# Optimization experiments

Hardware: AMD Instinct MI355X
Metric: run time of the kernel (lower is better)

The kernel has to match this reference:

```python
import jax, jax.numpy as jnp
import numpy as np

B, S, D, H = 4, 2048, 512, 8
HD = D // H


def setup_inputs() -> dict:
    key = jax.random.key(0)
    ks = jax.random.split(key, 12)
    x = jax.random.normal(ks[0], (B, S, D), dtype=jnp.float32)
    docking_scores = jax.random.uniform(ks[1], (B, S), dtype=jnp.float32)
    mask = jax.random.randint(ks[2], (B, S), 0, 2).astype(jnp.bool_)
    s = 0.02
    Wq = jax.random.normal(ks[3], (D, D), dtype=jnp.float32) * s
    bq = jnp.zeros((D,), dtype=jnp.float32)
    Wk = jax.random.normal(ks[4], (D, D), dtype=jnp.float32) * s
    bk = jnp.zeros((D,), dtype=jnp.float32)
    Wv = jax.random.normal(ks[5], (D, D), dtype=jnp.float32) * s
    bv = jnp.zeros((D,), dtype=jnp.float32)
    Wo = jax.random.normal(ks[6], (D, D), dtype=jnp.float32) * s
    bo = jnp.zeros((D,), dtype=jnp.float32)
    alpha = jnp.float32(0.5)
    beta = jnp.float32(0.5)
    return {"x": x, "docking_scores": docking_scores, "mask": mask,
            "Wq": Wq, "bq": bq, "Wk": Wk, "bk": bk, "Wv": Wv, "bv": bv,
            "Wo": Wo, "bo": bo, "alpha": alpha, "beta": beta}


def reference(x, docking_scores, mask, Wq, bq, Wk, bk, Wv, bv, Wo, bo, alpha, beta):
    # daa_type == ATTENTION: attention + docking-score blend (alpha unused here).
    b, s, d = x.shape
    # zero docking scores at padded positions; shape (B, S, 1)
    ds = jnp.where(mask[..., None], docking_scores[..., None], 0.0)
    def proj(W, bias):
        return (jnp.einsum('bsd,ed->bse', x, W) + bias).reshape(b, s, H, HD).transpose(0, 2, 1, 3)
    Q = proj(Wq, bq)  # (B, H, S, HD)
    K = proj(Wk, bk)
    V = proj(Wv, bv)
    scores = jnp.einsum('bhqd,bhkd->bhqk', Q, K) / jnp.sqrt(jnp.float32(HD))
    scores = jnp.where(mask[:, None, None, :], scores, -jnp.inf)  # key-padding mask
    attn = jax.nn.softmax(scores, axis=-1)  # (B, H, S, S)
    # docking blend: (B,1,S,1) broadcasts over heads and key dim (faithful to torch expand)
    attn = (1.0 - beta) * attn + beta * ds[:, None, :, :]
    ctx = jnp.einsum('bhqk,bhkd->bhqd', attn, V)
    ctx = ctx.transpose(0, 2, 1, 3).reshape(b, s, d)
    return jnp.einsum('bsd,od->bso', ctx, Wo) + bo
```

## Files before the change

kernel.cpp:

```cpp
#include <hip/hip_runtime.h>
#include <hip/hip_bf16.h>

#define B_ 4
#define S_ 2048
#define D_ 512
#define H_ 8
#define HD_ 64

typedef unsigned int uint;
typedef unsigned short ushort_t;
typedef __attribute__((ext_vector_type(4))) float f32x4;
typedef __attribute__((ext_vector_type(8))) short bf16x8;

#if __has_builtin(__builtin_amdgcn_exp2f)
#define EXP2F __builtin_amdgcn_exp2f
#else
#define EXP2F exp2f
#endif

__device__ __forceinline__ float bf2f(unsigned short u){ union{uint i;float f;}c; c.i = (uint)u<<16; return c.f; }
__device__ __forceinline__ unsigned short f2bf(float f){
    __hip_bfloat16 h = __float2bfloat16(f);
    return *reinterpret_cast<unsigned short*>(&h);
}

__device__ __forceinline__ void gload16(const unsigned short* g, const ushort_t* l){
    __builtin_amdgcn_global_load_lds(
        (const __attribute__((address_space(1))) unsigned int*)g,
        (__attribute__((address_space(3))) unsigned int*)l, 16, 0, 0);
}

__global__ __launch_bounds__(256) void convert_all(
    const float* __restrict__ x,
    const float* __restrict__ Wq, const float* __restrict__ Wk,
    const float* __restrict__ Wv, const float* __restrict__ Wo,
    ushort_t* __restrict__ xb, ushort_t* __restrict__ Wqkvb, ushort_t* __restrict__ Wob)
{
    const int NX = 1048576;
    const int NW = 65536;
    const int total = NX + 4 * NW;
    for (int i = blockIdx.x * 256 + threadIdx.x; i < total; i += gridDim.x * 256) {
        const float* src; ushort_t* dst; int so, dofs;
        if (i < NX) { src = x; so = i; dst = xb; dofs = i; }
        else if (i < NX + 3 * NW) {
            int j = i - NX;
            if (j < NW)          { src = Wq; so = j; }
            else if (j < 2 * NW) { src = Wk; so = j - NW; }
            else                 { src = Wv; so = j - 2 * NW; }
            dst = Wqkvb; dofs = j;
        } else { int k = i - NX - 3 * NW; src = Wo; so = k; dst = Wob; dofs = k; }
        float4 v = ((const float4*)src)[so];
        ushort4 u;
        u.x = f2bf(v.x); u.y = f2bf(v.y); u.z = f2bf(v.z); u.w = f2bf(v.w);
        ((ushort4*)dst)[dofs] = u;
    }
}

template<int MODE>
__global__ __launch_bounds__(256) void gemm_mfma(
    const ushort_t* __restrict__ A, const ushort_t* __restrict__ Bw,
    const float* __restrict__ b0, const float* __restrict__ b1, const float* __restrict__ b2,
    ushort_t* __restrict__ O0, ushort_t* __restrict__ O1, ushort_t* __restrict__ O2,
    float* __restrict__ Of)
{
    __shared__ __align__(16) unsigned char smem[34816];
    ushort_t* sA = (ushort_t*)smem;
    ushort_t* sB = sA + 8192;

    const int t = threadIdx.x, w = t >> 6, l = t & 63, g = l >> 4, c = l & 15;
    const int wm = w >> 1, wn = w & 1;
    const int row0 = blockIdx.y * 128, col0 = blockIdx.x * 128;

    const ushort_t* aSrc[4]; const ushort_t* bSrc[4];
    ushort_t* aDst[4]; ushort_t* bDst[4];
    #pragma unroll
    for (int i = 0; i < 4; ++i) {
        int cc = i * 256 + t;
        int row = cc >> 3, slot = (cc & 7) ^ (row & 7);
        aSrc[i] = A  + (size_t)(row0 + row) * 512 + slot * 8;
        bSrc[i] = Bw + (size_t)(col0 + row) * 512 + slot * 8;
        aDst[i] = sA + (i * 256 + w * 64) * 8;
        bDst[i] = sB + (i * 256 + w * 64) * 8;
    }

    f32x4 acc[4][4];
    #pragma unroll
    for (int mi = 0; mi < 4; ++mi)
        #pragma unroll
        for (int ni = 0; ni < 4; ++ni) acc[mi][ni] = (f32x4)0.f;

    for (int ks = 0; ks < 8; ++ks) {
        #pragma unroll
        for (int i = 0; i < 4; ++i) {
            gload16(aSrc[i], aDst[i]);
            gload16(bSrc[i], bDst[i]);
        }
        __syncthreads();
        #pragma unroll
        for (int kh = 0; kh < 2; ++kh) {
            bf16x8 af[4], bfv[4];
            const int sw = (((kh << 2) | g) ^ (c & 7)) << 3;
            #pragma unroll
            for (int mi = 0; mi < 4; ++mi)
                af[mi] = *(const bf16x8*)&sA[(wm * 64 + mi * 16 + c) * 64 + sw];
            #pragma unroll
            for (int ni = 0; ni < 4; ++ni)
                bfv[ni] = *(const bf16x8*)&sB[(wn * 64 + ni * 16 + c) * 64 + sw];
            #pragma unroll
            for (int mi = 0; mi < 4; ++mi)
                #pragma unroll
                for (int ni = 0; ni < 4; ++ni)
                    acc[mi][ni] = __builtin_amdgcn_mfma_f32_16x16x32_bf16(af[mi], bfv[ni], acc[mi][ni], 0, 0, 0);
        }
        #pragma unroll
        for (int i = 0; i < 4; ++i) { aSrc[i] += 64; bSrc[i] += 64; }
        __syncthreads();
    }

    if (MODE == 1) {
        #pragma unroll
        for (int mi = 0; mi < 4; ++mi)
            #pragma unroll
            for (int ni = 0; ni < 4; ++ni) {
                int n = col0 + wn * 64 + ni * 16 + c;
                float bias = b0[n];
                #pragma unroll
                for (int r = 0; r < 4; ++r)
                    Of[(size_t)(row0 + wm * 64 + mi * 16 + 4 * g + r) * 512 + n] =
                        acc[mi][ni][r] + bias;
            }
    } else {
        const int which = col0 >> 9;
        const float* bias = which == 0 ? b0 : (which == 1 ? b1 : b2);
        ushort_t (*Cl)[136] = (ushort_t(*)[136])smem;
        if (which < 2) {
            #pragma unroll
            for (int mi = 0; mi < 4; ++mi)
                #pragma unroll
                for (int ni = 0; ni < 4; ++ni) {
                    int n = wn * 64 + ni * 16 + c;
                    float bb = bias[(col0 & 511) + n];
                    #pragma unroll
                    for (int r = 0; r < 4; ++r)
                        Cl[wm * 64 + mi * 16 + 4 * g + r][n] = f2bf(acc[mi][ni][r] + bb);
                }
        } else {
            #pragma unroll
            for (int mi = 0; mi < 4; ++mi)
                #pragma unroll
                for (int ni = 0; ni < 4; ++ni) {
                    int n = wn * 64 + ni * 16 + c;
                    float bb = bias[(col0 & 511) + n];
                    #pragma unroll
                    for (int r = 0; r < 4; ++r)
                        Cl[n][wm * 64 + mi * 16 + 4 * g + r] = f2bf(acc[mi][ni][r] + bb);
                }
        }
        __syncthreads();
        const int r = t >> 1, half = t & 1;
        const int b = row0 >> 11;
        if (which < 2) {
            ushort_t* Out = which == 0 ? O0 : O1;
            int s = (row0 & 2047) + r;
            int e = (col0 & 511) + half * 64;
            int h = e >> 6;
            ushort_t* dst = Out + (((size_t)(b * 8 + h) * 2048 + s) << 6);
            #pragma unroll
            for (int j = 0; j < 8; ++j)
                *(bf16x8*)(dst + j * 8) = *(const bf16x8*)&Cl[r][half * 64 + j * 8];
        } else {
            int e = (col0 & 511) + r;
            int h = e >> 6, d = e & 63;
            int s0 = (row0 & 2047) + half * 64;
            ushort_t* dst = O2 + ((size_t)(b * 8 + h) * 64 + d) * 2048 + s0;
            #pragma unroll
            for (int j = 0; j < 8; ++j)
                *(bf16x8*)(dst + j * 8) = *(const bf16x8*)&Cl[r][half * 64 + j * 8];
        }
    }
}

__global__ __launch_bounds__(256) void vsum2(
    const __hip_bfloat16* __restrict__ Vt, float* __restrict__ Vsum)
{
    const int row = blockIdx.x * 4 + (threadIdx.x >> 6);
    const int l = threadIdx.x & 63;
    const unsigned short* p = (const unsigned short*)Vt + (size_t)row * S_;
    float s = 0.f;
    #pragma unroll
    for (int i = 0; i < 4; ++i) {
        uint4 u = *(const uint4*)(p + i * 512 + l * 8);
        s += bf2f((unsigned short)(u.x & 0xffff)) + bf2f((unsigned short)(u.x >> 16));
        s += bf2f((unsigned short)(u.y & 0xffff)) + bf2f((unsigned short)(u.y >> 16));
        s += bf2f((unsigned short)(u.z & 0xffff)) + bf2f((unsigned short)(u.z >> 16));
        s += bf2f((unsigned short)(u.w & 0xffff)) + bf2f((unsigned short)(u.w >> 16));
    }
    #pragma unroll
    for (int m = 1; m < 64; m <<= 1) s += __shfl_xor(s, m);
    if (l == 0) Vsum[row] = s;
}

__global__ __launch_bounds__(256, 2) void attn_mfma(
    const __hip_bfloat16* __restrict__ Qb, const __hip_bfloat16* __restrict__ Kb,
    const __hip_bfloat16* __restrict__ Vt, const float* __restrict__ Vsum,
    const float* __restrict__ dock, const int* __restrict__ mask,
    const float* __restrict__ beta_p, ushort_t* __restrict__ ctxb)
{
    __shared__ __align__(16) unsigned char smem[59392];
    ushort_t* Kbuf = (ushort_t*)smem;
    ushort_t* Vbuf = (ushort_t*)(smem + 16384);
    ushort_t (*Plds)[32][72] = (ushort_t(*)[32][72])(smem + 32768);
    float* mbias = (float*)(smem + 51200);
    float (*ctxl)[32][68] = (float(*)[32][68])smem;

    const int flat = blockIdx.x;
    const int xcd = flat & 7, idx = flat >> 3;
    const int bh = ((idx >> 4) << 3) + xcd;
    const int qtile = idx & 15;
    const int b = bh >> 3, h = bh & 7;
    const int t = threadIdx.x, w = t >> 6, l = t & 63;
    const int g = l >> 4, c = l & 15;
    const int q0 = qtile * 128 + w * 32;
    const float beta = beta_p[0];
    const ushort_t* Kp = (const ushort_t*)Kb + (size_t)bh * S_ * HD_;
    const ushort_t* Vp = (const ushort_t*)Vt + (size_t)bh * HD_ * S_;

    int koff[2], voff[2];
    const ushort_t* kdst[2]; const ushort_t* vdst[2];
    {
        const int srow = t >> 3, sslot = t & 7;
        #pragma unroll
        for (int ch = 0; ch < 2; ++ch) {
            int row = ch * 32 + srow;
            int sl = ((sslot ^ (row & 7))) * 8;
            koff[ch] = row * 64 + sl;
            voff[ch] = row * 2048 + sl;
            kdst[ch] = Kbuf + (ch * 256 + w * 64) * 8;
            vdst[ch] = Vbuf + (ch * 256 + w * 64) * 8;
        }
    }
#define STAGE(PAR, K0N) do {                                                    \
    _Pragma("unroll")                                                           \
    for (int ch = 0; ch < 2; ++ch) {                                            \
        gload16(Kp + (size_t)(K0N) * 64 + koff[ch], kdst[ch] + (PAR) * 4096);   \
        gload16(Vp + (K0N) + voff[ch],              vdst[ch] + (PAR) * 4096);   \
    }                                                                           \
} while (0)

    for (int i = t; i < 2048; i += 256)
        mbias[i] = mask[b * S_ + i] ? 0.f : -1e30f;
    STAGE(0, 0);

    bf16x8 qf[2][2];
    #pragma unroll
    for (int qt = 0; qt < 2; ++qt)
        #pragma unroll
        for (int ks = 0; ks < 2; ++ks) {
            const unsigned short* qp = (const unsigned short*)Qb +
                ((size_t)bh * S_ + q0 + qt * 16 + c) * HD_ + ks * 32 + g * 8;
            bf16x8 raw = *(const bf16x8*)qp;
            bf16x8 sc8;
            #pragma unroll
            for (int j = 0; j < 8; ++j) {
                float f = bf2f((unsigned short)raw[j]) * 0.125f;
                sc8[j] = (short)f2bf(f);
            }
            qf[qt][ks] = sc8;
        }

    f32x4 cacc[2][4];
    #pragma unroll
    for (int qt = 0; qt < 2; ++qt)
        #pragma unroll
        for (int dt = 0; dt < 4; ++dt) cacc[qt][dt] = (f32x4)0.f;
    float l_[2] = {0.f, 0.f};

    const int fsw0 = (g ^ (c & 7)) * 8;
    const int fsw1 = ((4 | g) ^ (c & 7)) * 8;

    __syncthreads();

    for (int k0 = 0, par = 0; k0 < S_; k0 += 64, par ^= 1) {
        if (k0 + 64 < S_) STAGE(par ^ 1, k0 + 64);
        const ushort_t* KB = Kbuf + par * 4096;
        const ushort_t* VB = Vbuf + par * 4096;

        bf16x8 kf[8];
        #pragma unroll
        for (int kt = 0; kt < 4; ++kt) {
            const ushort_t* kr = KB + (kt * 16 + c) * 64;
            kf[kt * 2]     = *(const bf16x8*)(kr + fsw0);
            kf[kt * 2 + 1] = *(const bf16x8*)(kr + fsw1);
        }
        bf16x8 vf[8];
        #pragma unroll
        for (int dt = 0; dt < 4; ++dt) {
            const ushort_t* vr = VB + (dt * 16 + c) * 64;
            vf[dt * 2]     = *(const bf16x8*)(vr + fsw0);
            vf[dt * 2 + 1] = *(const bf16x8*)(vr + fsw1);
        }

        f32x4 sacc[2][4];
        #pragma unroll
        for (int qt = 0; qt < 2; ++qt)
            #pragma unroll
            for (int kt = 0; kt < 4; ++kt) sacc[qt][kt] = (f32x4)0.f;
        __builtin_amdgcn_s_setprio(1);
        #pragma unroll
        for (int kt = 0; kt < 4; ++kt)
            #pragma unroll
            for (int qt = 0; qt < 2; ++qt) {
                sacc[qt][kt] = __builtin_amdgcn_mfma_f32_16x16x32_bf16(kf[kt * 2],     qf[qt][0], sacc[qt][kt], 0, 0, 0);
                sacc[qt][kt] = __builtin_amdgcn_mfma_f32_16x16x32_bf16(kf[kt * 2 + 1], qf[qt][1], sacc[qt][kt], 0, 0, 0);
            }
        __builtin_amdgcn_s_setprio(0);

        float mb_[4][4];
        #pragma unroll
        for (int kt = 0; kt < 4; ++kt)
            #pragma unroll
            for (int r = 0; r < 4; ++r)
                mb_[kt][r] = mbias[k0 + kt * 16 + g * 4 + r];

        #pragma unroll
        for (int qt = 0; qt < 2; ++qt) {
            float p_[16];
            float ps = 0.f;
            #pragma unroll
            for (int kt = 0; kt < 4; ++kt)
                #pragma unroll
                for (int r = 0; r < 4; ++r) {
                    float v = fmaf(sacc[qt][kt][r], 1.4426950408889634f, mb_[kt][r]);
                    float p = EXP2F(v);
                    p_[kt * 4 + r] = p;
                    ps += p;
                }
            l_[qt] += ps;
            #pragma unroll
            for (int kt = 0; kt < 4; ++kt) {
                uint lo = (uint)f2bf(p_[kt * 4 + 0]) | ((uint)f2bf(p_[kt * 4 + 1]) << 16);
                uint hi = (uint)f2bf(p_[kt * 4 + 2]) | ((uint)f2bf(p_[kt * 4 + 3]) << 16);
                *(uint2*)&Plds[w][16 * qt + c][kt * 16 + g * 4] = make_uint2(lo, hi);
            }
        }
        asm volatile("s_waitcnt lgkmcnt(0)" ::: "memory");
        __builtin_amdgcn_sched_barrier(0);

        bf16x8 pf[2][2];
        #pragma unroll
        for (int qt = 0; qt < 2; ++qt)
            #pragma unroll
            for (int ks = 0; ks < 2; ++ks)
                pf[qt][ks] = *(const bf16x8*)&Plds[w][16 * qt + c][ks * 32 + g * 8];
        __builtin_amdgcn_s_setprio(1);
        #pragma unroll
        for (int dt = 0; dt < 4; ++dt)
            #pragma unroll
            for (int qt = 0; qt < 2; ++qt) {
                cacc[qt][dt] = __builtin_amdgcn_mfma_f32_16x16x32_bf16(vf[dt * 2],     pf[qt][0], cacc[qt][dt], 0, 0, 0);
                cacc[qt][dt] = __builtin_amdgcn_mfma_f32_16x16x32_bf16(vf[dt * 2 + 1], pf[qt][1], cacc[qt][dt], 0, 0, 0);
            }
        __builtin_amdgcn_s_setprio(0);
        __syncthreads();
    }
#undef STAGE

    #pragma unroll
    for (int qt = 0; qt < 2; ++qt) {
        l_[qt] += __shfl_xor(l_[qt], 16);
        l_[qt] += __shfl_xor(l_[qt], 32);
    }

    __syncthreads();

    #pragma unroll
    for (int qt = 0; qt < 2; ++qt) {
        int qg = q0 + 16 * qt + c;
        float w1 = (1.f - beta) / l_[qt];
        float dq = (mask[b * S_ + qg] ? dock[b * S_ + qg] : 0.f) * beta;
        #pragma unroll
        for (int dt = 0; dt < 4; ++dt)
            #pragma unroll
            for (int r = 0; r < 4; ++r) {
                int d = dt * 16 + g * 4 + r;
                ctxl[w][16 * qt + c][d] = cacc[qt][dt][r] * w1 + dq * Vsum[bh * 64 + d];
            }
    }
    asm volatile("s_waitcnt lgkmcnt(0)" ::: "memory");
    __builtin_amdgcn_sched_barrier(0);
    {
        const int qloc = l >> 1, half = l & 1;
        const int qg = q0 + qloc;
        ushort_t* cp = ctxb + ((size_t)(b * 2048 + qg)) * 512 + h * 64 + half * 32;
        #pragma unroll
        for (int j = 0; j < 4; ++j) {
            float4 v0 = *(const float4*)&ctxl[w][qloc][half * 32 + j * 8];
            float4 v1 = *(const float4*)&ctxl[w][qloc][half * 32 + j * 8 + 4];
            bf16x8 u;
            u[0] = (short)f2bf(v0.x); u[1] = (short)f2bf(v0.y);
            u[2] = (short)f2bf(v0.z); u[3] = (short)f2bf(v0.w);
            u[4] = (short)f2bf(v1.x); u[5] = (short)f2bf(v1.y);
            u[6] = (short)f2bf(v1.z); u[7] = (short)f2bf(v1.w);
            *(bf16x8*)(cp + j * 8) = u;
        }
    }
}

extern "C" void kernel_launch(void* const* d_in, const int* in_sizes, int n_in,
                              void* d_out, int out_size, void* d_ws, size_t ws_size,
                              hipStream_t stream)
{
    const float* x    = (const float*)d_in[0];
    const float* dock = (const float*)d_in[1];
    const int*   mask = (const int*)d_in[2];
    const float* Wq   = (const float*)d_in[3];
    const float* bq   = (const float*)d_in[4];
    const float* Wk   = (const float*)d_in[5];
    const float* bk   = (const float*)d_in[6];
    const float* Wv   = (const float*)d_in[7];
    const float* bv   = (const float*)d_in[8];
    const float* Wo   = (const float*)d_in[9];
    const float* bo   = (const float*)d_in[10];
    const float* beta = (const float*)d_in[12];
    float* out = (float*)d_out;

    const size_t nqkv = (size_t)B_ * H_ * S_ * HD_;
    ushort_t* xb    = (ushort_t*)d_ws;
    ushort_t* Qb    = xb + nqkv;
    ushort_t* Kb    = Qb + nqkv;
    ushort_t* Vt    = Kb + nqkv;
    ushort_t* Wqkvb = Vt + nqkv;
    ushort_t* Wob   = Wqkvb + 1536 * 512;
    float*    Vsum  = (float*)(Wob + 512 * 512);
    ushort_t* ctxb  = xb;

    convert_all<<<1280, 256, 0, stream>>>(x, Wq, Wk, Wv, Wo, xb, Wqkvb, Wob);
    gemm_mfma<0><<<dim3(12, 64), 256, 0, stream>>>(xb, Wqkvb, bq, bk, bv, Qb, Kb, Vt, nullptr);
    vsum2<<<512, 256, 0, stream>>>((const __hip_bfloat16*)Vt, Vsum);
    attn_mfma<<<512, 256, 0, stream>>>(
        (const __hip_bfloat16*)Qb, (const __hip_bfloat16*)Kb, (const __hip_bfloat16*)Vt,
        Vsum, dock, mask, beta, ctxb);
    gemm_mfma<1><<<dim3(4, 64), 256, 0, stream>>>(ctxb, Wob, bo, nullptr, nullptr,
                                                  nullptr, nullptr, nullptr, out);
}
```

Measured before the change: 108.8 us.

## Switch attention to 32x32x16 MFMA with register-resident P and global mask bias

Rewrites the attention inner loop to use 32x32x16 bf16 MFMAs. The S accumulator layout now matches the B-operand layout of the PV MFMA, so P stays in registers and no longer round-trips through LDS. The 1/sqrt(d) scale is folded into the exp2 constant instead of pre-scaling Q, and the mask bias is precomputed once in the convert kernel and read from global memory, which shrinks LDS use. The risks are higher register pressure from the 16-wide accumulators, and V fragments now need split 8-byte LDS reads with possible bank conflicts.

```diff
diff --git a/kernel.cpp b/kernel.cpp
--- a/kernel.cpp
+++ b/kernel.cpp
@@ -10,6 +10,7 @@
 typedef unsigned int uint;
 typedef unsigned short ushort_t;
 typedef __attribute__((ext_vector_type(4))) float f32x4;
+typedef __attribute__((ext_vector_type(16))) float f32x16;
 typedef __attribute__((ext_vector_type(8))) short bf16x8;
 
 #if __has_builtin(__builtin_amdgcn_exp2f)
@@ -34,7 +35,9 @@
     const float* __restrict__ x,
     const float* __restrict__ Wq, const float* __restrict__ Wk,
     const float* __restrict__ Wv, const float* __restrict__ Wo,
-    ushort_t* __restrict__ xb, ushort_t* __restrict__ Wqkvb, ushort_t* __restrict__ Wob)
+    const int* __restrict__ mask,
+    ushort_t* __restrict__ xb, ushort_t* __restrict__ Wqkvb, ushort_t* __restrict__ Wob,
+    float* __restrict__ mbg)
 {
     const int NX = 1048576;
     const int NW = 65536;
@@ -54,6 +57,15 @@
         u.x = f2bf(v.x); u.y = f2bf(v.y); u.z = f2bf(v.z); u.w = f2bf(v.w);
         ((ushort4*)dst)[dofs] = u;
     }
+    for (int i = blockIdx.x * 256 + threadIdx.x; i < 2048; i += gridDim.x * 256) {
+        int4 mv = ((const int4*)mask)[i];
+        float4 o;
+        o.x = mv.x ? 0.f : -1e30f;
+        o.y = mv.y ? 0.f : -1e30f;
+        o.z = mv.z ? 0.f : -1e30f;
+        o.w = mv.w ? 0.f : -1e30f;
+        ((float4*)mbg)[i] = o;
+    }
 }
 
 template<int MODE>
@@ -204,26 +216,26 @@
     const __hip_bfloat16* __restrict__ Qb, const __hip_bfloat16* __restrict__ Kb,
     const __hip_bfloat16* __restrict__ Vt, const float* __restrict__ Vsum,
     const float* __restrict__ dock, const int* __restrict__ mask,
-    const float* __restrict__ beta_p, ushort_t* __restrict__ ctxb)
+    const float* __restrict__ mbg, const float* __restrict__ beta_p,
+    ushort_t* __restrict__ ctxb)
 {
-    __shared__ __align__(16) unsigned char smem[59392];
+    __shared__ __align__(16) unsigned char smem[35328];
     ushort_t* Kbuf = (ushort_t*)smem;
     ushort_t* Vbuf = (ushort_t*)(smem + 16384);
-    ushort_t (*Plds)[32][72] = (ushort_t(*)[32][72])(smem + 32768);
-    float* mbias = (float*)(smem + 51200);
-    float (*ctxl)[32][68] = (float(*)[32][68])smem;
 
     const int flat = blockIdx.x;
     const int xcd = flat & 7, idx = flat >> 3;
     const int bh = ((idx >> 4) << 3) + xcd;
     const int qtile = idx & 15;
-    const int b = bh >> 3, h = bh & 7;
-    const int t = threadIdx.x, w = t >> 6, l = t & 63;
-    const int g = l >> 4, c = l & 15;
+    const int b = bh >> 3, h8 = bh & 7;
+    const int t = threadIdx.x, w = t >> 6, lam = t & 63;
+    const int lq = lam & 31, hf = lam >> 5;
     const int q0 = qtile * 128 + w * 32;
+    const int qg = q0 + lq;
     const float beta = beta_p[0];
     const ushort_t* Kp = (const ushort_t*)Kb + (size_t)bh * S_ * HD_;
     const ushort_t* Vp = (const ushort_t*)Vt + (size_t)bh * HD_ * S_;
+    const float* mbp = mbg + b * S_;
 
     int koff[2], voff[2];
     const ushort_t* kdst[2]; const ushort_t* vdst[2];
@@ -232,7 +244,7 @@
         #pragma unroll
         for (int ch = 0; ch < 2; ++ch) {
             int row = ch * 32 + srow;
-            int sl = ((sslot ^ (row & 7))) * 8;
+            int sl = (sslot ^ (row & 7)) * 8;
             koff[ch] = row * 64 + sl;
             voff[ch] = row * 2048 + sl;
             kdst[ch] = Kbuf + (ch * 256 + w * 64) * 8;
@@ -247,36 +259,19 @@
     }                                                                           \
 } while (0)
 
-    for (int i = t; i < 2048; i += 256)
-        mbias[i] = mask[b * S_ + i] ? 0.f : -1e30f;
     STAGE(0, 0);
 
-    bf16x8 qf[2][2];
+    bf16x8 qf[4];
     #pragma unroll
-    for (int qt = 0; qt < 2; ++qt)
-        #pragma unroll
-        for (int ks = 0; ks < 2; ++ks) {
-            const unsigned short* qp = (const unsigned short*)Qb +
-                ((size_t)bh * S_ + q0 + qt * 16 + c) * HD_ + ks * 32 + g * 8;
-            bf16x8 raw = *(const bf16x8*)qp;
-            bf16x8 sc8;
-            #pragma unroll
-            for (int j = 0; j < 8; ++j) {
-                float f = bf2f((unsigned short)raw[j]) * 0.125f;
-                sc8[j] = (short)f2bf(f);
-            }
-            qf[qt][ks] = sc8;
-        }
-
-    f32x4 cacc[2][4];
-    #pragma unroll
-    for (int qt = 0; qt < 2; ++qt)
-        #pragma unroll
-        for (int dt = 0; dt < 4; ++dt) cacc[qt][dt] = (f32x4)0.f;
-    float l_[2] = {0.f, 0.f};
-
-    const int fsw0 = (g ^ (c & 7)) * 8;
-    const int fsw1 = ((4 | g) ^ (c & 7)) * 8;
+    for (int hd = 0; hd < 4; ++hd)
+        qf[hd] = *(const bf16x8*)((const ushort_t*)Qb +
+                 ((size_t)bh * S_ + qg) * HD_ + hd * 16 + hf * 8);
+
+    f32x16 cacc[2];
+    cacc[0] = (f32x16)0.f;
+    cacc[1] = (f32x16)0.f;
+    float l_ = 0.f;
+    const float CSC = 0.18033688011112042f;
 
     __syncthreads();
 
@@ -285,113 +280,95 @@
         const ushort_t* KB = Kbuf + par * 4096;
         const ushort_t* VB = Vbuf + par * 4096;
 
-        bf16x8 kf[8];
-        #pragma unroll
-        for (int kt = 0; kt < 4; ++kt) {
-            const ushort_t* kr = KB + (kt * 16 + c) * 64;
-            kf[kt * 2]     = *(const bf16x8*)(kr + fsw0);
-            kf[kt * 2 + 1] = *(const bf16x8*)(kr + fsw1);
-        }
-        bf16x8 vf[8];
-        #pragma unroll
-        for (int dt = 0; dt < 4; ++dt) {
-            const ushort_t* vr = VB + (dt * 16 + c) * 64;
-            vf[dt * 2]     = *(const bf16x8*)(vr + fsw0);
-            vf[dt * 2 + 1] = *(const bf16x8*)(vr + fsw1);
-        }
-
-        f32x4 sacc[2][4];
-        #pragma unroll
-        for (int qt = 0; qt < 2; ++qt)
-            #pragma unroll
-            for (int kt = 0; kt < 4; ++kt) sacc[qt][kt] = (f32x4)0.f;
+        f32x16 sacc[2];
+        sacc[0] = (f32x16)0.f;
+        sacc[1] = (f32x16)0.f;
         __builtin_amdgcn_s_setprio(1);
         #pragma unroll
-        for (int kt = 0; kt < 4; ++kt)
-            #pragma unroll
-            for (int qt = 0; qt < 2; ++qt) {
-                sacc[qt][kt] = __builtin_amdgcn_mfma_f32_16x16x32_bf16(kf[kt * 2],     qf[qt][0], sacc[qt][kt], 0, 0, 0);
-                sacc[qt][kt] = __builtin_amdgcn_mfma_f32_16x16x32_bf16(kf[kt * 2 + 1], qf[qt][1], sacc[qt][kt], 0, 0, 0);
+        for (int kt2 = 0; kt2 < 2; ++kt2) {
+            const int krow = kt2 * 32 + lq;
+            const ushort_t* kr = KB + krow * 64;
+            const int krs = krow & 7;
+            #pragma unroll
+            for (int hd = 0; hd < 4; ++hd) {
+                bf16x8 kf = *(const bf16x8*)(kr + ((((hd << 1) | hf) ^ krs) << 3));
+                sacc[kt2] = __builtin_amdgcn_mfma_f32_32x32x16_bf16(kf, qf[hd], sacc[kt2], 0, 0, 0);
             }
+        }
         __builtin_amdgcn_s_setprio(0);
 
-        float mb_[4][4];
-        #pragma unroll
-        for (int kt = 0; kt < 4; ++kt)
-            #pragma unroll
-            for (int r = 0; r < 4; ++r)
-                mb_[kt][r] = mbias[k0 + kt * 16 + g * 4 + r];
-
-        #pragma unroll
-        for (int qt = 0; qt < 2; ++qt) {
-            float p_[16];
-            float ps = 0.f;
-            #pragma unroll
-            for (int kt = 0; kt < 4; ++kt)
-                #pragma unroll
-                for (int r = 0; r < 4; ++r) {
-                    float v = fmaf(sacc[qt][kt][r], 1.4426950408889634f, mb_[kt][r]);
-                    float p = EXP2F(v);
-                    p_[kt * 4 + r] = p;
-                    ps += p;
+        float p[2][16];
+        #pragma unroll
+        for (int kt2 = 0; kt2 < 2; ++kt2) {
+            #pragma unroll
+            for (int qd = 0; qd < 4; ++qd) {
+                float4 mb = *(const float4*)(mbp + k0 + kt2 * 32 + qd * 8 + hf * 4);
+                float pv0 = EXP2F(fmaf(sacc[kt2][qd * 4 + 0], CSC, mb.x));
+                float pv1 = EXP2F(fmaf(sacc[kt2][qd * 4 + 1], CSC, mb.y));
+                float pv2 = EXP2F(fmaf(sacc[kt2][qd * 4 + 2], CSC, mb.z));
+                float pv3 = EXP2F(fmaf(sacc[kt2][qd * 4 + 3], CSC, mb.w));
+                p[kt2][qd * 4 + 0] = pv0; p[kt2][qd * 4 + 1] = pv1;
+                p[kt2][qd * 4 + 2] = pv2; p[kt2][qd * 4 + 3] = pv3;
+                l_ += pv0 + pv1 + pv2 + pv3;
+            }
+        }
+
+        __builtin_amdgcn_s_setprio(1);
+        #pragma unroll
+        for (int kt2 = 0; kt2 < 2; ++kt2) {
+            #pragma unroll
+            for (int ks = 0; ks < 2; ++ks) {
+                bf16x8 pf;
+                #pragma unroll
+                for (int m = 0; m < 8; ++m)
+                    pf[m] = (short)f2bf(p[kt2][ks * 8 + m]);
+                const int gB = (kt2 << 2) + (ks << 1);
+                #pragma unroll
+                for (int dt = 0; dt < 2; ++dt) {
+                    const int vrow = dt * 32 + lq;
+                    const int vrs = vrow & 7;
+                    const ushort_t* vr = VB + vrow * 64;
+                    uint2 lo = *(const uint2*)(vr + (((gB    ) ^ vrs) << 3) + (hf << 2));
+                    uint2 hi = *(const uint2*)(vr + (((gB + 1) ^ vrs) << 3) + (hf << 2));
+                    union { bf16x8 v; uint4 u; } cv;
+                    cv.u = make_uint4(lo.x, lo.y, hi.x, hi.y);
+                    cacc[dt] = __builtin_amdgcn_mfma_f32_32x32x16_bf16(cv.v, pf, cacc[dt], 0, 0, 0);
                 }
-            l_[qt] += ps;
-            #pragma unroll
-            for (int kt = 0; kt < 4; ++kt) {
-                uint lo = (uint)f2bf(p_[kt * 4 + 0]) | ((uint)f2bf(p_[kt * 4 + 1]) << 16);
-                uint hi = (uint)f2bf(p_[kt * 4 + 2]) | ((uint)f2bf(p_[kt * 4 + 3]) << 16);
-                *(uint2*)&Plds[w][16 * qt + c][kt * 16 + g * 4] = make_uint2(lo, hi);
             }
         }
-        asm volatile("s_waitcnt lgkmcnt(0)" ::: "memory");
-        __builtin_amdgcn_sched_barrier(0);
-
-        bf16x8 pf[2][2];
-        #pragma unroll
-        for (int qt = 0; qt < 2; ++qt)
-            #pragma unroll
-            for (int ks = 0; ks < 2; ++ks)
-                pf[qt][ks] = *(const bf16x8*)&Plds[w][16 * qt + c][ks * 32 + g * 8];
-        __builtin_amdgcn_s_setprio(1);
-        #pragma unroll
-        for (int dt = 0; dt < 4; ++dt)
-            #pragma unroll
-            for (int qt = 0; qt < 2; ++qt) {
-                cacc[qt][dt] = __builtin_amdgcn_mfma_f32_16x16x32_bf16(vf[dt * 2],     pf[qt][0], cacc[qt][dt], 0, 0, 0);
-                cacc[qt][dt] = __builtin_amdgcn_mfma_f32_16x16x32_bf16(vf[dt * 2 + 1], pf[qt][1], cacc[qt][dt], 0, 0, 0);
-            }
         __builtin_amdgcn_s_setprio(0);
         __syncthreads();
     }
 #undef STAGE
 
-    #pragma unroll
-    for (int qt = 0; qt < 2; ++qt) {
-        l_[qt] += __shfl_xor(l_[qt], 16);
-        l_[qt] += __shfl_xor(l_[qt], 32);
-    }
+    l_ += __shfl_xor(l_, 32);
 
     __syncthreads();
 
-    #pragma unroll
-    for (int qt = 0; qt < 2; ++qt) {
-        int qg = q0 + 16 * qt + c;
-        float w1 = (1.f - beta) / l_[qt];
+    float (*ctxl)[32][68] = (float(*)[32][68])smem;
+    {
+        float w1 = (1.f - beta) / l_;
         float dq = (mask[b * S_ + qg] ? dock[b * S_ + qg] : 0.f) * beta;
         #pragma unroll
-        for (int dt = 0; dt < 4; ++dt)
-            #pragma unroll
-            for (int r = 0; r < 4; ++r) {
-                int d = dt * 16 + g * 4 + r;
-                ctxl[w][16 * qt + c][d] = cacc[qt][dt][r] * w1 + dq * Vsum[bh * 64 + d];
+        for (int dt = 0; dt < 2; ++dt)
+            #pragma unroll
+            for (int qd = 0; qd < 4; ++qd) {
+                int d0 = dt * 32 + qd * 8 + hf * 4;
+                float4 vs = *(const float4*)(Vsum + bh * 64 + d0);
+                float4 o;
+                o.x = cacc[dt][qd * 4 + 0] * w1 + dq * vs.x;
+                o.y = cacc[dt][qd * 4 + 1] * w1 + dq * vs.y;
+                o.z = cacc[dt][qd * 4 + 2] * w1 + dq * vs.z;
+                o.w = cacc[dt][qd * 4 + 3] * w1 + dq * vs.w;
+                *(float4*)&ctxl[w][lq][d0] = o;
             }
     }
     asm volatile("s_waitcnt lgkmcnt(0)" ::: "memory");
     __builtin_amdgcn_sched_barrier(0);
     {
-        const int qloc = l >> 1, half = l & 1;
-        const int qg = q0 + qloc;
-        ushort_t* cp = ctxb + ((size_t)(b * 2048 + qg)) * 512 + h * 64 + half * 32;
+        const int qloc = lam >> 1, half = lam & 1;
+        const int qg2 = q0 + qloc;
+        ushort_t* cp = ctxb + ((size_t)(b * 2048 + qg2)) * 512 + h8 * 64 + half * 32;
         #pragma unroll
         for (int j = 0; j < 4; ++j) {
             float4 v0 = *(const float4*)&ctxl[w][qloc][half * 32 + j * 8];
@@ -432,14 +409,15 @@
     ushort_t* Wqkvb = Vt + nqkv;
     ushort_t* Wob   = Wqkvb + 1536 * 512;
     float*    Vsum  = (float*)(Wob + 512 * 512);
+    float*    mbg   = Vsum + 2048;
     ushort_t* ctxb  = xb;
 
-    convert_all<<<1280, 256, 0, stream>>>(x, Wq, Wk, Wv, Wo, xb, Wqkvb, Wob);
+    convert_all<<<1280, 256, 0, stream>>>(x, Wq, Wk, Wv, Wo, mask, xb, Wqkvb, Wob, mbg);
     gemm_mfma<0><<<dim3(12, 64), 256, 0, stream>>>(xb, Wqkvb, bq, bk, bv, Qb, Kb, Vt, nullptr);
     vsum2<<<512, 256, 0, stream>>>((const __hip_bfloat16*)Vt, Vsum);
     attn_mfma<<<512, 256, 0, stream>>>(
         (const __hip_bfloat16*)Qb, (const __hip_bfloat16*)Kb, (const __hip_bfloat16*)Vt,
-        Vsum, dock, mask, beta, ctxb);
+        Vsum, dock, mask, mbg, beta, ctxb);
     gemm_mfma<1><<<dim3(4, 64), 256, 0, stream>>>(ctxb, Wob, bo, nullptr, nullptr,
                                                   nullptr, nullptr, nullptr, out);
 }
```

After: 122.3 us. 1.12x slower.
